# Optimization experiments

Measured on AMD Instinct MI355X. Metric: run time of the kernel, lower is better.

The kernel has to match this reference:

```python
import jax, jax.numpy as jnp
import numpy as np

TRAJ_LEN = 11
MAX_INNER = 64          # fixed cap on adaptive steps per save interval (masked when done)
RTOL, ATOL = 1e-3, 1e-6
DT0 = 1e-3
B, D, HID = 4096, 64, 32

# Tsit5 Butcher tableau (Tsitouras 2011)
A21 = 0.161
A31, A32 = -0.008480655492356989, 0.335480655492357
A41, A42, A43 = 2.8971530571054935, -6.359448489975075, 4.3622954328695815
A51, A52, A53, A54 = 5.325864828439257, -11.748883564062828, 7.4955393428898365, -0.09249506636175525
A61, A62, A63, A64, A65 = 5.86145544294642, -12.92096931784711, 8.159367898576159, -0.071584973281401, -0.028269050394068383
B1, B2, B3, B4, B5, B6 = 0.09646076681806523, 0.01, 0.4798896504144996, 1.379008574103742, -3.290069515436081, 2.324710524099774
E1, E2, E3, E4, E5, E6, E7 = (-0.00178001105222577714, -0.0008164344596567469, 0.007880878010261995,
                              -0.1447110071732629, 0.5823571654525552, -0.45808210592918697, 0.015151515151515152)


def _mlp(W1, b1, W2, b2, W3, b3, y):
    h = jax.nn.softplus(W1 @ y + b1)
    h = jax.nn.softplus(W2 @ h + b2)
    return W3 @ h + b3


def _integrate(params, y0, ts):
    f = lambda y: _mlp(*params, y)

    def inner(state, _):
        t, y, dt, n = state
        remaining = ts_dummy = None  # placeholder removed below
        return state, None

    def make_inner(t_target):
        def inner(state, _):
            t, y, dt, n = state
            remaining = t_target - t
            done = remaining <= 1e-12
            h = jnp.minimum(dt, jnp.maximum(remaining, 0.0))
            k1 = f(y)
            k2 = f(y + h * (A21 * k1))
            k3 = f(y + h * (A31 * k1 + A32 * k2))
            k4 = f(y + h * (A41 * k1 + A42 * k2 + A43 * k3))
            k5 = f(y + h * (A51 * k1 + A52 * k2 + A53 * k3 + A54 * k4))
            k6 = f(y + h * (A61 * k1 + A62 * k2 + A63 * k3 + A64 * k4 + A65 * k5))
            y5 = y + h * (B1 * k1 + B2 * k2 + B3 * k3 + B4 * k4 + B5 * k5 + B6 * k6)
            k7 = f(y5)
            err = h * (E1 * k1 + E2 * k2 + E3 * k3 + E4 * k4 + E5 * k5 + E6 * k6 + E7 * k7)
            scale = ATOL + RTOL * jnp.maximum(jnp.abs(y), jnp.abs(y5))
            enorm = jnp.maximum(jnp.sqrt(jnp.mean((err / scale) ** 2)), 1e-10)
            accept = enorm <= 1.0
            fac = jnp.clip(0.9 * enorm ** -0.2, 0.1, 5.0)
            step_ok = accept & ~done
            t_n = jnp.where(step_ok, t + h, t)
            y_n = jnp.where(step_ok, y5, y)
            dt_n = jnp.where(done, dt, jnp.maximum(h * fac, 1e-8))
            n_n = n + jnp.where(done, jnp.int32(0), jnp.int32(1))
            return (t_n, y_n, dt_n, n_n), None
        return jax.checkpoint(inner)

    def interval(carry, t_target):
        carry, _ = jax.lax.scan(make_inner(t_target), carry, None, length=MAX_INNER)
        return carry, carry[1]

    init = (ts[0], y0, jnp.asarray(DT0, y0.dtype), jnp.int32(0))
    (tf, yf, dtf, n), ys = jax.lax.scan(interval, init, ts[1:])
    traj = jnp.concatenate([y0[None], ys], axis=0)  # [TRAJ_LEN, D]
    return traj, n


def setup_inputs() -> dict:
    key = jax.random.key(0)
    ks = jax.random.split(key, 7)
    u = lambda k, shape, fan_in: jax.random.uniform(k, shape, jnp.float32, -1.0, 1.0) / np.sqrt(fan_in)
    return {
        "x0s": jax.random.normal(ks[0], (B, D), jnp.float32),
        "W1": u(ks[1], (HID, D), D), "b1": u(ks[2], (HID,), D),
        "W2": u(ks[3], (HID, HID), HID), "b2": u(ks[4], (HID,), HID),
        "W3": u(ks[5], (D, HID), HID), "b3": u(ks[6], (D,), HID),
        "T": 10,
    }


def reference(x0s, W1, b1, W2, b2, W3, b3, T):
    ts = jnp.linspace(0.0, float(T), TRAJ_LEN).astype(x0s.dtype)
    params = (W1, b1, W2, b2, W3, b3)
    trajs, ns = jax.vmap(lambda y0: _integrate(params, y0, ts))(x0s)
    return trajs, jnp.sum(ns)
```

## Files before the change

### kernel.cpp

```cpp
#include <hip/hip_runtime.h>
#include <math.h>

#define A21f 0.161f
#define A31f -0.008480655492356989f
#define A32f 0.335480655492357f
#define A41f 2.8971530571054935f
#define A42f -6.359448489975075f
#define A43f 4.3622954328695815f
#define A51f 5.325864828439257f
#define A52f -11.748883564062828f
#define A53f 7.4955393428898365f
#define A54f -0.09249506636175525f
#define A61f 5.86145544294642f
#define A62f -12.92096931784711f
#define A63f 8.159367898576159f
#define A64f -0.071584973281401f
#define A65f -0.028269050394068383f
#define B1f 0.09646076681806523f
#define B2f 0.01f
#define B3f 0.4798896504144996f
#define B4f 1.379008574103742f
#define B5f -3.290069515436081f
#define B6f 2.324710524099774f
#define E1f -0.00178001105222577714f
#define E2f -0.0008164344596567469f
#define E3f 0.007880878010261995f
#define E4f -0.1447110071732629f
#define E5f 0.5823571654525552f
#define E6f -0.45808210592918697f
#define E7f 0.015151515151515152f

#define WPB 4

#define FMAC_RR(acc, v, w, N)                                              \
    asm("v_fmac_f32_dpp %0, %1, %2 row_ror:" #N " row_mask:0xf bank_mask:0xf" \
        : "+v"(acc) : "v"(v), "v"(w))

#define DOT16(acc, W, v) do {            \
    acc = fmaf((W)[0], (v), acc);        \
    FMAC_RR(acc, v, (W)[1], 1);          \
    FMAC_RR(acc, v, (W)[2], 2);          \
    FMAC_RR(acc, v, (W)[3], 3);          \
    FMAC_RR(acc, v, (W)[4], 4);          \
    FMAC_RR(acc, v, (W)[5], 5);          \
    FMAC_RR(acc, v, (W)[6], 6);          \
    FMAC_RR(acc, v, (W)[7], 7);          \
    FMAC_RR(acc, v, (W)[8], 8);          \
    FMAC_RR(acc, v, (W)[9], 9);          \
    FMAC_RR(acc, v, (W)[10], 10);        \
    FMAC_RR(acc, v, (W)[11], 11);        \
    FMAC_RR(acc, v, (W)[12], 12);        \
    FMAC_RR(acc, v, (W)[13], 13);        \
    FMAC_RR(acc, v, (W)[14], 14);        \
    FMAC_RR(acc, v, (W)[15], 15);        \
} while (0)

__device__ __forceinline__ float sp(float x) {
    float t = exp2f(-fabsf(x) * 1.44269504088896341f);
    return fmaxf(x, 0.0f) + 0.69314718055994531f * __log2f(1.0f + t);
}

__global__ __launch_bounds__(256)
__attribute__((amdgpu_waves_per_eu(4, 4)))
void ode_kernel(const float* __restrict__ x0s,
                const float* __restrict__ W1, const float* __restrict__ b1,
                const float* __restrict__ W2, const float* __restrict__ b2,
                const float* __restrict__ W3, const float* __restrict__ b3,
                const void* __restrict__ Tptr,
                float* __restrict__ out, int out_size, int B)
{
    const int wave = threadIdx.x >> 6;
    const int lane = threadIdx.x & 63;
    const int traj = blockIdx.x * WPB + wave;
    if (traj >= B) return;

    const int p = lane & 15;
    const int g = lane >> 4;
    const int godd = g & 1;
    const int jh = g >> 1;

    float W1a[16], W1b[16], W2r[16], W3a[16], W3b[16];
    const int r2 = p + 16 * godd;
#pragma unroll
    for (int k = 0; k < 16; ++k) {
        const int c = (p + k) & 15;
        W1a[k] = W1[p * 64 + 16 * g + c];
        W1b[k] = W1[(16 + p) * 64 + 16 * g + c];
        W2r[k] = W2[r2 * 32 + 16 * jh + c];
        W3a[k] = W3[lane * 32 + c];
        W3b[k] = W3[lane * 32 + 16 + c];
    }
#pragma unroll
    for (int k = 0; k < 16; ++k) {
        asm("" : "+v"(W1a[k]));
        asm("" : "+v"(W1b[k]));
        asm("" : "+v"(W2r[k]));
        asm("" : "+v"(W3a[k]));
        asm("" : "+v"(W3b[k]));
    }
    const float b1a = b1[p], b1b = b1[p + 16];
    const float b2r = b2[r2], b3r = b3[lane];

    auto f = [&](float u) -> float {
        float a1a = 0.f, a1b = 0.f;
        DOT16(a1a, W1a, u);
        DOT16(a1b, W1b, u);
        a1a += __shfl_xor(a1a, 16);
        a1a += __shfl_xor(a1a, 32);
        a1b += __shfl_xor(a1b, 16);
        a1b += __shfl_xor(a1b, 32);
        float h1A = sp(a1a + b1a);
        float h1B = sp(a1b + b1b);
        float S = jh ? h1B : h1A;
        float a2 = 0.f;
        DOT16(a2, W2r, S);
        a2 += __shfl_xor(a2, 32);
        float h2v = sp(a2 + b2r);
        float other = __shfl_xor(h2v, 16);
        float h2A = godd ? other : h2v;
        float h2B = godd ? h2v : other;
        float a3 = 0.f;
        DOT16(a3, W3a, h2A);
        DOT16(a3, W3b, h2B);
        return a3 + b3r;
    };

    int ti = *(const int*)Tptr;
    float Tf = (ti > 0 && ti < 1000000) ? (float)ti : *(const float*)Tptr;
    const float ts_step = Tf / 10.0f;

    float y = x0s[traj * 64 + lane];
    out[traj * 704 + lane] = y;

    float t = 0.0f;
    float dt = 1e-3f;
    int n = 0;

    float k1 = f(y);

    for (int iv = 1; iv <= 10; ++iv) {
        const float t_target = (iv == 10) ? Tf : ts_step * (float)iv;
        for (int it = 0; it < 64; ++it) {
            const float remaining = t_target - t;
            if (remaining <= 1e-12f) break;
            const float h = fminf(dt, fmaxf(remaining, 0.0f));

            float k2 = f(y + h * (A21f * k1));
            float k3 = f(y + h * (A31f * k1 + A32f * k2));
            float k4 = f(y + h * (A41f * k1 + A42f * k2 + A43f * k3));
            float k5 = f(y + h * (A51f * k1 + A52f * k2 + A53f * k3 + A54f * k4));
            float k6 = f(y + h * (A61f * k1 + A62f * k2 + A63f * k3 + A64f * k4 + A65f * k5));
            float y5 = y + h * (B1f * k1 + B2f * k2 + B3f * k3 + B4f * k4 + B5f * k5 + B6f * k6);
            float k7 = f(y5);
            float err = h * (E1f * k1 + E2f * k2 + E3f * k3 + E4f * k4 + E5f * k5 + E6f * k6 + E7f * k7);

            float scale = 1e-6f + 1e-3f * fmaxf(fabsf(y), fabsf(y5));
            float r = err / scale;
            float s = r * r;
#pragma unroll
            for (int m = 32; m >= 1; m >>= 1) s += __shfl_xor(s, m);
            float enorm = fmaxf(sqrtf(s * (1.0f / 64.0f)), 1e-10f);

            bool accept = enorm <= 1.0f;
            float fac = 0.9f * exp2f(-0.2f * __log2f(enorm));
            fac = fminf(fmaxf(fac, 0.1f), 5.0f);

            if (accept) { t += h; y = y5; k1 = k7; }
            dt = fmaxf(h * fac, 1e-8f);
            ++n;
        }
        out[traj * 704 + iv * 64 + lane] = y;
    }

    if (lane == 0) atomicAdd(out + (out_size - 1), (float)n);
}

__global__ void init_n(float* p) { *p = 0.0f; }

extern "C" void kernel_launch(void* const* d_in, const int* in_sizes, int n_in,
                              void* d_out, int out_size, void* d_ws, size_t ws_size,
                              hipStream_t stream) {
    const float* x0s = (const float*)d_in[0];
    const float* W1  = (const float*)d_in[1];
    const float* b1  = (const float*)d_in[2];
    const float* W2  = (const float*)d_in[3];
    const float* b2  = (const float*)d_in[4];
    const float* W3  = (const float*)d_in[5];
    const float* b3  = (const float*)d_in[6];
    const void*  Tp  = d_in[7];
    float* out = (float*)d_out;

    const int B = in_sizes[0] / 64;
    const int grid = (B + WPB - 1) / WPB;

    init_n<<<1, 1, 0, stream>>>(out + (out_size - 1));
    ode_kernel<<<grid, 256, 0, stream>>>(x0s, W1, b1, W2, b2, W3, b3, Tp,
                                         out, out_size, B);
}
```

Measured before the change: 191.3 us.

## Replicate ODE state per 16-lane row to cut cross-row shuffles in MLP

Changes the lane layout so each 16-lane DPP row holds the full 64-dim state as four values per lane. The layer-1 reduction and the error-norm reduction now run entirely inside a row with DPP row_ror adds, dropping the xor-32 shuffles. The aim is to shorten the latency of the serial RK stage chain. The cost is redundant work: lane groups 0/2 and 1/3 compute identical hidden units, so per-lane FMA count roughly doubles. Register-resident weights grow from 80 to 160 VGPRs, and the waves-per-EU hint is relaxed to allow that, which risks lower occupancy.

After: 453.7 us. 2.37x slower.

```diff
diff --git a/kernel.cpp b/kernel.cpp
--- a/kernel.cpp
+++ b/kernel.cpp
@@ -36,7 +36,11 @@
     asm("v_fmac_f32_dpp %0, %1, %2 row_ror:" #N " row_mask:0xf bank_mask:0xf" \
         : "+v"(acc) : "v"(v), "v"(w))
 
-#define DOT16(acc, W, v) do {            \
+#define ADD_RR(s, N)                                                       \
+    asm("v_add_f32_dpp %0, %1, %0 row_ror:" #N " row_mask:0xf bank_mask:0xf" \
+        : "+v"(s) : "v"(s))
+
+#define DOT16F(acc, W, v) do {           \
     acc = fmaf((W)[0], (v), acc);        \
     FMAC_RR(acc, v, (W)[1], 1);          \
     FMAC_RR(acc, v, (W)[2], 2);          \
@@ -61,7 +65,7 @@
 }
 
 __global__ __launch_bounds__(256)
-__attribute__((amdgpu_waves_per_eu(4, 4)))
+__attribute__((amdgpu_waves_per_eu(1, 4)))
 void ode_kernel(const float* __restrict__ x0s,
                 const float* __restrict__ W1, const float* __restrict__ b1,
                 const float* __restrict__ W2, const float* __restrict__ b2,
@@ -74,69 +78,90 @@
     const int traj = blockIdx.x * WPB + wave;
     if (traj >= B) return;
 
-    const int p = lane & 15;
-    const int g = lane >> 4;
-    const int godd = g & 1;
-    const int jh = g >> 1;
-
-    float W1a[16], W1b[16], W2r[16], W3a[16], W3b[16];
-    const int r2 = p + 16 * godd;
+    const int p  = lane & 15;
+    const int g  = lane >> 4;
+    const int ga = g & 1;
+
+    const int o1 = 16 * ga + p;
+    const int c0 = o1;
+    const int c1 = 32 + o1;
+
+    float W1L[4][16], W2L[2][16], W3L[2][2][16];
 #pragma unroll
     for (int k = 0; k < 16; ++k) {
         const int c = (p + k) & 15;
-        W1a[k] = W1[p * 64 + 16 * g + c];
-        W1b[k] = W1[(16 + p) * 64 + 16 * g + c];
-        W2r[k] = W2[r2 * 32 + 16 * jh + c];
-        W3a[k] = W3[lane * 32 + c];
-        W3b[k] = W3[lane * 32 + 16 + c];
+        W1L[0][k] = W1[o1 * 64 + c];
+        W1L[1][k] = W1[o1 * 64 + 16 + c];
+        W1L[2][k] = W1[o1 * 64 + 32 + c];
+        W1L[3][k] = W1[o1 * 64 + 48 + c];
+        W2L[0][k] = W2[o1 * 32 + c];
+        W2L[1][k] = W2[o1 * 32 + 16 + c];
+        W3L[0][0][k] = W3[c0 * 32 + c];
+        W3L[0][1][k] = W3[c0 * 32 + 16 + c];
+        W3L[1][0][k] = W3[c1 * 32 + c];
+        W3L[1][1][k] = W3[c1 * 32 + 16 + c];
     }
 #pragma unroll
     for (int k = 0; k < 16; ++k) {
-        asm("" : "+v"(W1a[k]));
-        asm("" : "+v"(W1b[k]));
-        asm("" : "+v"(W2r[k]));
-        asm("" : "+v"(W3a[k]));
-        asm("" : "+v"(W3b[k]));
-    }
-    const float b1a = b1[p], b1b = b1[p + 16];
-    const float b2r = b2[r2], b3r = b3[lane];
-
-    auto f = [&](float u) -> float {
-        float a1a = 0.f, a1b = 0.f;
-        DOT16(a1a, W1a, u);
-        DOT16(a1b, W1b, u);
-        a1a += __shfl_xor(a1a, 16);
-        a1a += __shfl_xor(a1a, 32);
-        a1b += __shfl_xor(a1b, 16);
-        a1b += __shfl_xor(a1b, 32);
-        float h1A = sp(a1a + b1a);
-        float h1B = sp(a1b + b1b);
-        float S = jh ? h1B : h1A;
-        float a2 = 0.f;
-        DOT16(a2, W2r, S);
-        a2 += __shfl_xor(a2, 32);
-        float h2v = sp(a2 + b2r);
-        float other = __shfl_xor(h2v, 16);
-        float h2A = godd ? other : h2v;
-        float h2B = godd ? h2v : other;
-        float a3 = 0.f;
-        DOT16(a3, W3a, h2A);
-        DOT16(a3, W3b, h2B);
-        return a3 + b3r;
+        asm("" : "+v"(W1L[0][k]), "+v"(W1L[1][k]), "+v"(W1L[2][k]), "+v"(W1L[3][k]));
+        asm("" : "+v"(W2L[0][k]), "+v"(W2L[1][k]));
+        asm("" : "+v"(W3L[0][0][k]), "+v"(W3L[0][1][k]), "+v"(W3L[1][0][k]), "+v"(W3L[1][1][k]));
+    }
+    const float b1L = b1[o1], b2L = b2[o1];
+    const float b3c0 = b3[c0], b3c1 = b3[c1];
+
+    auto f = [&](const float* u, float* r) {
+        float a0 = 0.f, a1 = 0.f, a2 = 0.f, a3 = 0.f;
+        DOT16F(a0, W1L[0], u[0]);
+        DOT16F(a1, W1L[1], u[1]);
+        DOT16F(a2, W1L[2], u[2]);
+        DOT16F(a3, W1L[3], u[3]);
+        float h1 = sp(((a0 + a1) + (a2 + a3)) + b1L);
+        float oth = __shfl_xor(h1, 16);
+        float hA = ga ? oth : h1;
+        float hB = ga ? h1 : oth;
+        float s0 = 0.f, s1 = 0.f;
+        DOT16F(s0, W2L[0], hA);
+        DOT16F(s1, W2L[1], hB);
+        float h2 = sp((s0 + s1) + b2L);
+        float oth2 = __shfl_xor(h2, 16);
+        float gA = ga ? oth2 : h2;
+        float gB = ga ? h2 : oth2;
+        float t00 = 0.f, t01 = 0.f, t10 = 0.f, t11 = 0.f;
+        DOT16F(t00, W3L[0][0], gA);
+        DOT16F(t01, W3L[0][1], gB);
+        DOT16F(t10, W3L[1][0], gA);
+        DOT16F(t11, W3L[1][1], gB);
+        float rc0 = (t00 + t01) + b3c0;
+        float rc1 = (t10 + t11) + b3c1;
+        float e0 = __shfl_xor(rc0, 16);
+        float e1 = __shfl_xor(rc1, 16);
+        r[0] = ga ? e0 : rc0;
+        r[1] = ga ? rc0 : e0;
+        r[2] = ga ? e1 : rc1;
+        r[3] = ga ? rc1 : e1;
     };
 
     int ti = *(const int*)Tptr;
     float Tf = (ti > 0 && ti < 1000000) ? (float)ti : *(const float*)Tptr;
     const float ts_step = Tf / 10.0f;
 
-    float y = x0s[traj * 64 + lane];
-    out[traj * 704 + lane] = y;
+    float y[4];
+#pragma unroll
+    for (int q = 0; q < 4; ++q) y[q] = x0s[traj * 64 + 16 * q + p];
+
+    {
+        float lo = ga ? y[1] : y[0];
+        float hi = ga ? y[3] : y[2];
+        out[traj * 704 + lane] = (g & 2) ? hi : lo;
+    }
 
     float t = 0.0f;
     float dt = 1e-3f;
     int n = 0;
 
-    float k1 = f(y);
+    float k1v[4];
+    f(y, k1v);
 
     for (int iv = 1; iv <= 10; ++iv) {
         const float t_target = (iv == 10) ? Tf : ts_step * (float)iv;
@@ -145,31 +170,72 @@
             if (remaining <= 1e-12f) break;
             const float h = fminf(dt, fmaxf(remaining, 0.0f));
 
-            float k2 = f(y + h * (A21f * k1));
-            float k3 = f(y + h * (A31f * k1 + A32f * k2));
-            float k4 = f(y + h * (A41f * k1 + A42f * k2 + A43f * k3));
-            float k5 = f(y + h * (A51f * k1 + A52f * k2 + A53f * k3 + A54f * k4));
-            float k6 = f(y + h * (A61f * k1 + A62f * k2 + A63f * k3 + A64f * k4 + A65f * k5));
-            float y5 = y + h * (B1f * k1 + B2f * k2 + B3f * k3 + B4f * k4 + B5f * k5 + B6f * k6);
-            float k7 = f(y5);
-            float err = h * (E1f * k1 + E2f * k2 + E3f * k3 + E4f * k4 + E5f * k5 + E6f * k6 + E7f * k7);
-
-            float scale = 1e-6f + 1e-3f * fmaxf(fabsf(y), fabsf(y5));
-            float r = err / scale;
-            float s = r * r;
-#pragma unroll
-            for (int m = 32; m >= 1; m >>= 1) s += __shfl_xor(s, m);
+            float a[4], k2v[4], k3v[4], k4v[4], k5v[4], k6v[4], k7v[4], y5[4], ev[4];
+            const float c21 = h * A21f;
+#pragma unroll
+            for (int q = 0; q < 4; ++q) a[q] = fmaf(c21, k1v[q], y[q]);
+            f(a, k2v);
+            const float c31 = h * A31f, c32 = h * A32f;
+#pragma unroll
+            for (int q = 0; q < 4; ++q) a[q] = fmaf(c32, k2v[q], fmaf(c31, k1v[q], y[q]));
+            f(a, k3v);
+            const float c41 = h * A41f, c42 = h * A42f, c43 = h * A43f;
+#pragma unroll
+            for (int q = 0; q < 4; ++q)
+                a[q] = fmaf(c43, k3v[q], fmaf(c42, k2v[q], fmaf(c41, k1v[q], y[q])));
+            f(a, k4v);
+            const float c51 = h * A51f, c52 = h * A52f, c53 = h * A53f, c54 = h * A54f;
+#pragma unroll
+            for (int q = 0; q < 4; ++q)
+                a[q] = fmaf(c54, k4v[q], fmaf(c53, k3v[q], fmaf(c52, k2v[q], fmaf(c51, k1v[q], y[q]))));
+            f(a, k5v);
+            const float c61 = h * A61f, c62 = h * A62f, c63 = h * A63f, c64 = h * A64f, c65 = h * A65f;
+#pragma unroll
+            for (int q = 0; q < 4; ++q)
+                a[q] = fmaf(c65, k5v[q], fmaf(c64, k4v[q], fmaf(c63, k3v[q],
+                        fmaf(c62, k2v[q], fmaf(c61, k1v[q], y[q])))));
+            f(a, k6v);
+            const float d1 = h * B1f, d2 = h * B2f, d3 = h * B3f, d4 = h * B4f, d5 = h * B5f, d6 = h * B6f;
+#pragma unroll
+            for (int q = 0; q < 4; ++q)
+                y5[q] = fmaf(d6, k6v[q], fmaf(d5, k5v[q], fmaf(d4, k4v[q],
+                         fmaf(d3, k3v[q], fmaf(d2, k2v[q], fmaf(d1, k1v[q], y[q]))))));
+            f(y5, k7v);
+            const float e1c = h * E1f, e2c = h * E2f, e3c = h * E3f, e4c = h * E4f,
+                        e5c = h * E5f, e6c = h * E6f, e7c = h * E7f;
+            float s = 0.f;
+#pragma unroll
+            for (int q = 0; q < 4; ++q) {
+                ev[q] = fmaf(e7c, k7v[q], fmaf(e6c, k6v[q], fmaf(e5c, k5v[q],
+                         fmaf(e4c, k4v[q], fmaf(e3c, k3v[q], fmaf(e2c, k2v[q],
+                         e1c * k1v[q]))))));
+                float scl = 1e-6f + 1e-3f * fmaxf(fabsf(y[q]), fabsf(y5[q]));
+                float rr_ = ev[q] / scl;
+                s = fmaf(rr_, rr_, s);
+            }
+            ADD_RR(s, 8);
+            ADD_RR(s, 4);
+            ADD_RR(s, 2);
+            ADD_RR(s, 1);
             float enorm = fmaxf(sqrtf(s * (1.0f / 64.0f)), 1e-10f);
 
             bool accept = enorm <= 1.0f;
             float fac = 0.9f * exp2f(-0.2f * __log2f(enorm));
             fac = fminf(fmaxf(fac, 0.1f), 5.0f);
 
-            if (accept) { t += h; y = y5; k1 = k7; }
+            if (accept) {
+                t += h;
+#pragma unroll
+                for (int q = 0; q < 4; ++q) { y[q] = y5[q]; k1v[q] = k7v[q]; }
+            }
             dt = fmaxf(h * fac, 1e-8f);
             ++n;
         }
-        out[traj * 704 + iv * 64 + lane] = y;
+        {
+            float lo = ga ? y[1] : y[0];
+            float hi = ga ? y[3] : y[2];
+            out[traj * 704 + iv * 64 + lane] = (g & 2) ? hi : lo;
+        }
     }
 
     if (lane == 0) atomicAdd(out + (out_size - 1), (float)n);
```

## Integrate two trajectories per wave to interleave independent DPP dot chains

Applied to the files above, without the earlier changes.

Each wavefront now advances two trajectories together. Every MLP evaluation interleaves the two independent accumulation chains, split into low and high halves with separate accumulators, which shortens the serial dependency on DPP FMAs and shuffles. Occupancy is lowered to 2 waves per EU to leave room for the extra registers, and the grid is halved. The cost is lockstep divergence: the pair keeps stepping until both trajectories reach each target, so the faster one idles, and fewer waves are available to hide latency.

After: 200.5 us. +4.8%, slower.

```diff
diff --git a/kernel.cpp b/kernel.cpp
--- a/kernel.cpp
+++ b/kernel.cpp
@@ -36,7 +36,7 @@
     asm("v_fmac_f32_dpp %0, %1, %2 row_ror:" #N " row_mask:0xf bank_mask:0xf" \
         : "+v"(acc) : "v"(v), "v"(w))
 
-#define DOT16(acc, W, v) do {            \
+#define DOT8_LO(acc, W, v) do {          \
     acc = fmaf((W)[0], (v), acc);        \
     FMAC_RR(acc, v, (W)[1], 1);          \
     FMAC_RR(acc, v, (W)[2], 2);          \
@@ -45,6 +45,8 @@
     FMAC_RR(acc, v, (W)[5], 5);          \
     FMAC_RR(acc, v, (W)[6], 6);          \
     FMAC_RR(acc, v, (W)[7], 7);          \
+} while (0)
+#define DOT8_HI(acc, W, v) do {          \
     FMAC_RR(acc, v, (W)[8], 8);          \
     FMAC_RR(acc, v, (W)[9], 9);          \
     FMAC_RR(acc, v, (W)[10], 10);        \
@@ -61,7 +63,7 @@
 }
 
 __global__ __launch_bounds__(256)
-__attribute__((amdgpu_waves_per_eu(4, 4)))
+__attribute__((amdgpu_waves_per_eu(2, 2)))
 void ode_kernel(const float* __restrict__ x0s,
                 const float* __restrict__ W1, const float* __restrict__ b1,
                 const float* __restrict__ W2, const float* __restrict__ b2,
@@ -71,8 +73,11 @@
 {
     const int wave = threadIdx.x >> 6;
     const int lane = threadIdx.x & 63;
-    const int traj = blockIdx.x * WPB + wave;
-    if (traj >= B) return;
+    const int wid  = blockIdx.x * WPB + wave;
+    const int trA  = wid * 2;
+    const int trB  = wid * 2 + 1;
+    if (trA >= B) return;
+    const bool hasB = (trB < B);
 
     const int p = lane & 15;
     const int g = lane >> 4;
@@ -101,78 +106,157 @@
     const float b1a = b1[p], b1b = b1[p + 16];
     const float b2r = b2[r2], b3r = b3[lane];
 
-    auto f = [&](float u) -> float {
-        float a1a = 0.f, a1b = 0.f;
-        DOT16(a1a, W1a, u);
-        DOT16(a1b, W1b, u);
-        a1a += __shfl_xor(a1a, 16);
-        a1a += __shfl_xor(a1a, 32);
-        a1b += __shfl_xor(a1b, 16);
-        a1b += __shfl_xor(a1b, 32);
-        float h1A = sp(a1a + b1a);
-        float h1B = sp(a1b + b1b);
-        float S = jh ? h1B : h1A;
-        float a2 = 0.f;
-        DOT16(a2, W2r, S);
-        a2 += __shfl_xor(a2, 32);
-        float h2v = sp(a2 + b2r);
-        float other = __shfl_xor(h2v, 16);
-        float h2A = godd ? other : h2v;
-        float h2B = godd ? h2v : other;
-        float a3 = 0.f;
-        DOT16(a3, W3a, h2A);
-        DOT16(a3, W3b, h2B);
-        return a3 + b3r;
+    auto fd = [&](float uA, float uB, float& rA, float& rB) {
+        float aA0 = 0.f, aA1 = 0.f, aA2 = 0.f, aA3 = 0.f;
+        float aB0 = 0.f, aB1 = 0.f, aB2 = 0.f, aB3 = 0.f;
+        DOT8_LO(aA0, W1a, uA);
+        DOT8_LO(aB0, W1a, uB);
+        DOT8_HI(aA1, W1a, uA);
+        DOT8_HI(aB1, W1a, uB);
+        DOT8_LO(aA2, W1b, uA);
+        DOT8_LO(aB2, W1b, uB);
+        DOT8_HI(aA3, W1b, uA);
+        DOT8_HI(aB3, W1b, uB);
+        float a1aA = aA0 + aA1, a1bA = aA2 + aA3;
+        float a1aB = aB0 + aB1, a1bB = aB2 + aB3;
+        {
+            float t1 = __shfl_xor(a1aA, 16);
+            float t2 = __shfl_xor(a1bA, 16);
+            float t3 = __shfl_xor(a1aB, 16);
+            float t4 = __shfl_xor(a1bB, 16);
+            a1aA += t1; a1bA += t2; a1aB += t3; a1bB += t4;
+            t1 = __shfl_xor(a1aA, 32);
+            t2 = __shfl_xor(a1bA, 32);
+            t3 = __shfl_xor(a1aB, 32);
+            t4 = __shfl_xor(a1bB, 32);
+            a1aA += t1; a1bA += t2; a1aB += t3; a1bB += t4;
+        }
+        float h1AA = sp(a1aA + b1a);
+        float h1BA = sp(a1bA + b1b);
+        float h1AB = sp(a1aB + b1a);
+        float h1BB = sp(a1bB + b1b);
+        float SA = jh ? h1BA : h1AA;
+        float SB = jh ? h1BB : h1AB;
+        float a2A0 = 0.f, a2A1 = 0.f, a2B0 = 0.f, a2B1 = 0.f;
+        DOT8_LO(a2A0, W2r, SA);
+        DOT8_LO(a2B0, W2r, SB);
+        DOT8_HI(a2A1, W2r, SA);
+        DOT8_HI(a2B1, W2r, SB);
+        float a2A = a2A0 + a2A1;
+        float a2B = a2B0 + a2B1;
+        {
+            float t1 = __shfl_xor(a2A, 32);
+            float t2 = __shfl_xor(a2B, 32);
+            a2A += t1; a2B += t2;
+        }
+        float h2vA = sp(a2A + b2r);
+        float h2vB = sp(a2B + b2r);
+        float oA = __shfl_xor(h2vA, 16);
+        float oB = __shfl_xor(h2vB, 16);
+        float h2AA = godd ? oA : h2vA;
+        float h2BA = godd ? h2vA : oA;
+        float h2AB = godd ? oB : h2vB;
+        float h2BB = godd ? h2vB : oB;
+        float cA0 = 0.f, cA1 = 0.f, dA0 = 0.f, dA1 = 0.f;
+        float cB0 = 0.f, cB1 = 0.f, dB0 = 0.f, dB1 = 0.f;
+        DOT8_LO(cA0, W3a, h2AA);
+        DOT8_LO(cB0, W3a, h2AB);
+        DOT8_HI(cA1, W3a, h2AA);
+        DOT8_HI(cB1, W3a, h2AB);
+        DOT8_LO(dA0, W3b, h2BA);
+        DOT8_LO(dB0, W3b, h2BB);
+        DOT8_HI(dA1, W3b, h2BA);
+        DOT8_HI(dB1, W3b, h2BB);
+        rA = ((cA0 + cA1) + (dA0 + dA1)) + b3r;
+        rB = ((cB0 + cB1) + (dB0 + dB1)) + b3r;
     };
 
     int ti = *(const int*)Tptr;
     float Tf = (ti > 0 && ti < 1000000) ? (float)ti : *(const float*)Tptr;
     const float ts_step = Tf / 10.0f;
 
-    float y = x0s[traj * 64 + lane];
-    out[traj * 704 + lane] = y;
-
-    float t = 0.0f;
-    float dt = 1e-3f;
-    int n = 0;
-
-    float k1 = f(y);
+    float yA = x0s[trA * 64 + lane];
+    float yB = hasB ? x0s[trB * 64 + lane] : 0.0f;
+    out[trA * 704 + lane] = yA;
+    if (hasB) out[trB * 704 + lane] = yB;
+
+    float tA = 0.0f, tB = hasB ? 0.0f : Tf;
+    float dtA = 1e-3f, dtB = 1e-3f;
+    int nA = 0, nB = 0;
+
+    float k1A, k1B;
+    fd(yA, yB, k1A, k1B);
 
     for (int iv = 1; iv <= 10; ++iv) {
         const float t_target = (iv == 10) ? Tf : ts_step * (float)iv;
         for (int it = 0; it < 64; ++it) {
-            const float remaining = t_target - t;
-            if (remaining <= 1e-12f) break;
-            const float h = fminf(dt, fmaxf(remaining, 0.0f));
-
-            float k2 = f(y + h * (A21f * k1));
-            float k3 = f(y + h * (A31f * k1 + A32f * k2));
-            float k4 = f(y + h * (A41f * k1 + A42f * k2 + A43f * k3));
-            float k5 = f(y + h * (A51f * k1 + A52f * k2 + A53f * k3 + A54f * k4));
-            float k6 = f(y + h * (A61f * k1 + A62f * k2 + A63f * k3 + A64f * k4 + A65f * k5));
-            float y5 = y + h * (B1f * k1 + B2f * k2 + B3f * k3 + B4f * k4 + B5f * k5 + B6f * k6);
-            float k7 = f(y5);
-            float err = h * (E1f * k1 + E2f * k2 + E3f * k3 + E4f * k4 + E5f * k5 + E6f * k6 + E7f * k7);
-
-            float scale = 1e-6f + 1e-3f * fmaxf(fabsf(y), fabsf(y5));
-            float r = err / scale;
-            float s = r * r;
+            const float remA = t_target - tA;
+            const float remB = t_target - tB;
+            const bool actA = remA > 1e-12f;
+            const bool actB = remB > 1e-12f;
+            if (!actA && !actB) break;
+            const float hA = fminf(dtA, fmaxf(remA, 0.0f));
+            const float hB = fminf(dtB, fmaxf(remB, 0.0f));
+
+            float k2A, k2B, k3A, k3B, k4A, k4B, k5A, k5B, k6A, k6B, k7A, k7B;
+            float aA, aB;
+            aA = yA + hA * (A21f * k1A);
+            aB = yB + hB * (A21f * k1B);
+            fd(aA, aB, k2A, k2B);
+            aA = yA + hA * (A31f * k1A + A32f * k2A);
+            aB = yB + hB * (A31f * k1B + A32f * k2B);
+            fd(aA, aB, k3A, k3B);
+            aA = yA + hA * (A41f * k1A + A42f * k2A + A43f * k3A);
+            aB = yB + hB * (A41f * k1B + A42f * k2B + A43f * k3B);
+            fd(aA, aB, k4A, k4B);
+            aA = yA + hA * (A51f * k1A + A52f * k2A + A53f * k3A + A54f * k4A);
+            aB = yB + hB * (A51f * k1B + A52f * k2B + A53f * k3B + A54f * k4B);
+            fd(aA, aB, k5A, k5B);
+            aA = yA + hA * (A61f * k1A + A62f * k2A + A63f * k3A + A64f * k4A + A65f * k5A);
+            aB = yB + hB * (A61f * k1B + A62f * k2B + A63f * k3B + A64f * k4B + A65f * k5B);
+            fd(aA, aB, k6A, k6B);
+            float y5A = yA + hA * (B1f * k1A + B2f * k2A + B3f * k3A + B4f * k4A + B5f * k5A + B6f * k6A);
+            float y5B = yB + hB * (B1f * k1B + B2f * k2B + B3f * k3B + B4f * k4B + B5f * k5B + B6f * k6B);
+            fd(y5A, y5B, k7A, k7B);
+            float errA = hA * (E1f * k1A + E2f * k2A + E3f * k3A + E4f * k4A + E5f * k5A + E6f * k6A + E7f * k7A);
+            float errB = hB * (E1f * k1B + E2f * k2B + E3f * k3B + E4f * k4B + E5f * k5B + E6f * k6B + E7f * k7B);
+
+            float sclA = 1e-6f + 1e-3f * fmaxf(fabsf(yA), fabsf(y5A));
+            float sclB = 1e-6f + 1e-3f * fmaxf(fabsf(yB), fabsf(y5B));
+            float rA_ = errA / sclA;
+            float rB_ = errB / sclB;
+            float sA = rA_ * rA_;
+            float sB = rB_ * rB_;
 #pragma unroll
-            for (int m = 32; m >= 1; m >>= 1) s += __shfl_xor(s, m);
-            float enorm = fmaxf(sqrtf(s * (1.0f / 64.0f)), 1e-10f);
-
-            bool accept = enorm <= 1.0f;
-            float fac = 0.9f * exp2f(-0.2f * __log2f(enorm));
-            fac = fminf(fmaxf(fac, 0.1f), 5.0f);
-
-            if (accept) { t += h; y = y5; k1 = k7; }
-            dt = fmaxf(h * fac, 1e-8f);
-            ++n;
+            for (int m = 32; m >= 1; m >>= 1) {
+                float ta = __shfl_xor(sA, m);
+                float tb = __shfl_xor(sB, m);
+                sA += ta; sB += tb;
+            }
+            float enA = fmaxf(sqrtf(sA * (1.0f / 64.0f)), 1e-10f);
+            float enB = fmaxf(sqrtf(sB * (1.0f / 64.0f)), 1e-10f);
+
+            bool accA = enA <= 1.0f;
+            bool accB = enB <= 1.0f;
+            float facA = fminf(fmaxf(0.9f * exp2f(-0.2f * __log2f(enA)), 0.1f), 5.0f);
+            float facB = fminf(fmaxf(0.9f * exp2f(-0.2f * __log2f(enB)), 0.1f), 5.0f);
+
+            if (actA) {
+                if (accA) { tA += hA; yA = y5A; k1A = k7A; }
+                dtA = fmaxf(hA * facA, 1e-8f);
+                ++nA;
+            }
+            if (actB) {
+                if (accB) { tB += hB; yB = y5B; k1B = k7B; }
+                dtB = fmaxf(hB * facB, 1e-8f);
+                ++nB;
+            }
         }
-        out[traj * 704 + iv * 64 + lane] = y;
+        out[trA * 704 + iv * 64 + lane] = yA;
+        if (hasB) out[trB * 704 + iv * 64 + lane] = yB;
     }
 
-    if (lane == 0) atomicAdd(out + (out_size - 1), (float)n);
+    if (lane == 0) atomicAdd(out + (out_size - 1), (float)(nA + (hasB ? nB : 0)));
 }
 
 __global__ void init_n(float* p) { *p = 0.0f; }
@@ -191,7 +275,8 @@
     float* out = (float*)d_out;
 
     const int B = in_sizes[0] / 64;
-    const int grid = (B + WPB - 1) / WPB;
+    const int nwaves = (B + 1) / 2;
+    const int grid = (nwaves + WPB - 1) / WPB;
 
     init_n<<<1, 1, 0, stream>>>(out + (out_size - 1));
     ode_kernel<<<grid, 256, 0, stream>>>(x0s, W1, b1, W2, b2, W3, b3, Tp,
```
